# Kernel optimization log

Measured on AMD Instinct MI355X. Metric: run time of the kernel, lower is better.

The kernel has to match this reference:

```python
import jax, jax.numpy as jnp
import numpy as np

GRID_SIZE = 5       # efficient-KAN defaults
SPLINE_ORDER = 3
GRID_RANGE = (-1.0, 1.0)
N_BASIS = GRID_SIZE + SPLINE_ORDER  # 8
LN_EPS = 1e-5


def _make_grid(in_features):
    h = (GRID_RANGE[1] - GRID_RANGE[0]) / GRID_SIZE
    g = np.arange(-SPLINE_ORDER, GRID_SIZE + SPLINE_ORDER + 1, dtype=np.float32) * h + GRID_RANGE[0]
    return jnp.asarray(np.tile(g, (in_features, 1)))  # [in, G+2k+1]


def _b_splines(x, grid):
    # x: [N, in], grid: [in, G+2k+1] -> [N, in, G+k]
    x = x[..., None]
    bases = ((x >= grid[:, :-1]) & (x < grid[:, 1:])).astype(x.dtype)
    for k in range(1, SPLINE_ORDER + 1):
        bases = ((x - grid[:, : -(k + 1)]) / (grid[:, k:-1] - grid[:, : -(k + 1)]) * bases[..., :-1]
                 + (grid[:, k + 1:] - x) / (grid[:, k + 1:] - grid[:, 1:-k]) * bases[..., 1:])
    return bases


def _layer_norm(x, scale, bias):
    mu = jnp.mean(x, axis=-1, keepdims=True)
    var = jnp.mean(jnp.square(x - mu), axis=-1, keepdims=True)
    return (x - mu) * jax.lax.rsqrt(var + LN_EPS) * scale + bias


def setup_inputs() -> dict:
    key = jax.random.key(0)
    B, S, D = 2, 4096, 256
    IN = 3 * D
    ks = jax.random.split(key, 20)
    s = 0.02
    inp = {
        'axial_tokens': jax.random.normal(ks[0], (B, S, D), jnp.float32),
        'sagittal_tokens': jax.random.normal(ks[1], (B, S, D), jnp.float32),
        'coronal_tokens': jax.random.normal(ks[2], (B, S, D), jnp.float32),
        'wq': jax.random.normal(ks[3], (D, D), jnp.float32) * s,
        'bq': jnp.zeros((D,), jnp.float32),
        'wk': jax.random.normal(ks[4], (D, D), jnp.float32) * s,
        'bk': jnp.zeros((D,), jnp.float32),
        'wv': jax.random.normal(ks[5], (D, D), jnp.float32) * s,
        'bv': jnp.zeros((D,), jnp.float32),
        'view_emb': jax.random.normal(ks[6], (3, D), jnp.float32) * s,
        'ln_ax_scale': jnp.ones((D,), jnp.float32), 'ln_ax_bias': jnp.zeros((D,), jnp.float32),
        'ln_sg_scale': jnp.ones((D,), jnp.float32), 'ln_sg_bias': jnp.zeros((D,), jnp.float32),
        'ln_co_scale': jnp.ones((D,), jnp.float32), 'ln_co_bias': jnp.zeros((D,), jnp.float32),
        'base_weight': jax.random.normal(ks[7], (D, IN), jnp.float32) * s,
        'spline_weight': jax.random.normal(ks[8], (D, IN, N_BASIS), jnp.float32) * s,
        'spline_scaler': 1.0 + jax.random.normal(ks[9], (D, IN), jnp.float32) * 0.1,
    }
    return inp


def reference(axial_tokens, sagittal_tokens, coronal_tokens,
              wq, bq, wk, bk, wv, bv, view_emb,
              ln_ax_scale, ln_ax_bias, ln_sg_scale, ln_sg_bias, ln_co_scale, ln_co_bias,
              base_weight, spline_weight, spline_scaler):
    D = axial_tokens.shape[-1]
    inv_sqrt_d = 1.0 / jnp.sqrt(jnp.float32(D))

    def attend(tokens, emb, ln_s, ln_b):
        q = tokens @ wq.T + bq
        k = tokens @ wk.T + bk
        v = tokens @ wv.T + bv
        # torch adds q @ view_emb_row_broadcast^T: every column of the bias equals q . emb
        bias = (q @ emb)[..., None]                      # [B,S,1]
        scores = jnp.einsum('bqd,bkd->bqk', q, k) * inv_sqrt_d + bias
        w = jax.nn.softmax(scores, axis=-1)
        att = jnp.einsum('bqk,bkd->bqd', w, v)
        return _layer_norm(att + tokens, ln_s, ln_b)

    ax = attend(axial_tokens, view_emb[0], ln_ax_scale, ln_ax_bias)
    sg = attend(sagittal_tokens, view_emb[1], ln_sg_scale, ln_sg_bias)
    co = attend(coronal_tokens, view_emb[2], ln_co_scale, ln_co_bias)

    x = jnp.concatenate((ax, sg, co), axis=-1)          # [B,S,3D]
    B, S, IN = x.shape
    grid = _make_grid(IN)
    base = jax.nn.silu(x) @ base_weight.T               # [B,S,D]
    sb = _b_splines(x.reshape(-1, IN), grid)            # [B*S, IN, G+k]
    sw = spline_weight * spline_scaler[..., None]       # [D, IN, G+k]
    spline = jnp.einsum('nif,oif->no', sb, sw).reshape(B, S, -1)
    return base + spline
```

## Files before the change

kernel.cpp:

```cpp
#include <hip/hip_runtime.h>
#include <hip/hip_bf16.h>
#include <math.h>


typedef __hip_bfloat16 bf16;
using bf16x8 = __attribute__((ext_vector_type(8))) __bf16;
using f32x4  = __attribute__((ext_vector_type(4))) float;

__device__ __forceinline__ void load_lds16(const void* g, void* l) {
  __builtin_amdgcn_global_load_lds((__attribute__((address_space(1))) void*)g,
                                   (__attribute__((address_space(3))) void*)l,
                                   16, 0, 0);
}

__device__ __forceinline__ float wave_sum(float v) {
#pragma unroll
  for (int o = 32; o > 0; o >>= 1) v += __shfl_down(v, o, 64);
  return v;
}

template <typename OutT, bool EXP>
__global__ __launch_bounds__(256) void mfma_gemm_bt(
    const bf16* __restrict__ A, const bf16* __restrict__ B,
    const float* __restrict__ bias, OutT* __restrict__ C,
    float* __restrict__ lpart, int K, int lda, int ldb, int ldc, int zshift,
    size_t zAh, size_t zAl, size_t zBh, size_t zBl, size_t zC, float scale) {
  __shared__ __align__(16) bf16 As[4096];
  __shared__ __align__(16) bf16 Bs[4096];
  const int tid = (int)threadIdx.x;
  const int lane = tid & 63;
  const int w = tid >> 6;
  const int m0 = (int)blockIdx.y << 7;
  const int n0 = (int)blockIdx.x << 7;
  const size_t z = blockIdx.z;
  const size_t zlo = z & (((size_t)1 << zshift) - 1);
  A += (z >> zshift) * zAh + zlo * zAl;
  B += (z >> zshift) * zBh + zlo * zBl;
  C += z * zC;

  const int srow = lane >> 2;
  const int qg = (lane & 3) ^ ((lane >> 3) & 3);
  const int ci0 = w, ci1 = w + 4;
  const bf16* gA0 = A + (size_t)(m0 + ci0 * 16 + srow) * lda + qg * 8;
  const bf16* gA1 = A + (size_t)(m0 + ci1 * 16 + srow) * lda + qg * 8;
  const bf16* gB0 = B + (size_t)(n0 + ci0 * 16 + srow) * ldb + qg * 8;
  const bf16* gB1 = B + (size_t)(n0 + ci1 * 16 + srow) * ldb + qg * 8;
  bf16* lA0 = As + ci0 * 512;
  bf16* lA1 = As + ci1 * 512;
  bf16* lB0 = Bs + ci0 * 512;
  bf16* lB1 = Bs + ci1 * 512;

  const int m15 = lane & 15, quad = lane >> 4;
  const int fq = quad ^ ((m15 >> 1) & 3);
  const int aoff = m15 * 32 + fq * 8;
  const bf16* pA = As + ((w >> 1) << 11) + aoff;
  const bf16* pB = Bs + ((w & 1) << 11) + aoff;

  f32x4 acc[4][4];
#pragma unroll
  for (int mi = 0; mi < 4; ++mi)
#pragma unroll
    for (int ni = 0; ni < 4; ++ni) acc[mi][ni] = (f32x4)(0.0f);

  for (int k0 = 0; k0 < K; k0 += 32) {
    load_lds16(gA0, lA0);
    load_lds16(gA1, lA1);
    load_lds16(gB0, lB0);
    load_lds16(gB1, lB1);
    gA0 += 32; gA1 += 32; gB0 += 32; gB1 += 32;
    __syncthreads();
    bf16x8 av[4], bv[4];
#pragma unroll
    for (int i = 0; i < 4; ++i) {
      av[i] = *(const bf16x8*)(pA + i * 512);
      bv[i] = *(const bf16x8*)(pB + i * 512);
    }
#pragma unroll
    for (int mi = 0; mi < 4; ++mi)
#pragma unroll
      for (int ni = 0; ni < 4; ++ni)
        acc[mi][ni] = __builtin_amdgcn_mfma_f32_16x16x32_bf16(
            av[mi], bv[ni], acc[mi][ni], 0, 0, 0);
    __syncthreads();
  }

  const int crow = m0 + ((w >> 1) << 6) + quad * 4;
  const int ccol = n0 + ((w & 1) << 6) + m15;
  float rs[4][4] = {};
#pragma unroll
  for (int ni = 0; ni < 4; ++ni) {
    const int col = ccol + ni * 16;
    const float bb = bias ? bias[col] : 0.0f;
#pragma unroll
    for (int mi = 0; mi < 4; ++mi) {
#pragma unroll
      for (int i = 0; i < 4; ++i) {
        const int row = crow + mi * 16 + i;
        float v = acc[mi][ni][i] * scale + bb;
        if constexpr (EXP) {
          v = __expf(v);
          rs[mi][i] += v;
        }
        if constexpr (sizeof(OutT) == 2)
          C[(size_t)row * ldc + col] = __float2bfloat16(v);
        else
          C[(size_t)row * ldc + col] = v;
      }
    }
  }
  if constexpr (EXP) {
    const int ch = ((int)blockIdx.x << 1) | (w & 1);
#pragma unroll
    for (int mi = 0; mi < 4; ++mi)
#pragma unroll
      for (int i = 0; i < 4; ++i) {
        float sv = rs[mi][i];
        sv += __shfl_xor(sv, 1);
        sv += __shfl_xor(sv, 2);
        sv += __shfl_xor(sv, 4);
        sv += __shfl_xor(sv, 8);
        if (m15 == 0)
          lpart[(size_t)ch * 4096 + crow + mi * 16 + i] = sv;
      }
  }
}

__global__ __launch_bounds__(256) void resid_ln_kernel(
    const float* __restrict__ attp, const float* __restrict__ lpart,
    const float* __restrict__ tok, const float* __restrict__ gamma,
    const float* __restrict__ beta, float* __restrict__ x, int vIdx) {
  __shared__ float red[4];
  __shared__ float sinvl;
  const int n = (int)blockIdx.x;
  const int d = (int)threadIdx.x;
  const int b = n >> 12, r = n & 4095;
  float ls = 0.f;
  if (d < 64) ls = lpart[((size_t)(b * 64 + d)) * 4096 + r];
  ls = wave_sum(ls);
  if (d == 0) sinvl = 1.0f / ls;
  const size_t abase = (size_t)(b * 4) * 1048576 + (size_t)r * 256 + d;
  const float asum = attp[abase] + attp[abase + 1048576] +
                     attp[abase + 2097152] + attp[abase + 3145728];
  __syncthreads();
  const float y = asum * sinvl + tok[(size_t)n * 256 + d];
  float s = wave_sum(y);
  if ((d & 63) == 0) red[d >> 6] = s;
  __syncthreads();
  const float mu = (red[0] + red[1] + red[2] + red[3]) * (1.0f / 256.0f);
  __syncthreads();
  const float c = y - mu;
  float s2 = wave_sum(c * c);
  if ((d & 63) == 0) red[d >> 6] = s2;
  __syncthreads();
  const float var = (red[0] + red[1] + red[2] + red[3]) * (1.0f / 256.0f);
  const float rstd = rsqrtf(var + 1e-5f);
  x[(size_t)n * 768 + vIdx * 256 + d] = c * rstd * gamma[d] + beta[d];
}

__global__ __launch_bounds__(256) void prep_w(
    const float* __restrict__ bw, const float* __restrict__ sw,
    const float* __restrict__ scaler, bf16* __restrict__ Wmat) {
  const int o = blockIdx.x;
  for (int ii = 0; ii < 3; ++ii) {
    const int i = ii * 256 + (int)threadIdx.x;
    const float s = scaler[(size_t)o * 768 + i];
    bf16* p = Wmat + (size_t)o * 6912 + i * 9;
    const float* swp = sw + ((size_t)o * 768 + i) * 8;
#pragma unroll
    for (int f = 0; f < 8; ++f) p[f] = __float2bfloat16(swp[f] * s);
    p[8] = __float2bfloat16(bw[(size_t)o * 768 + i]);
  }
}

__global__ __launch_bounds__(256) void prep_qkvw(
    const float* __restrict__ wq, const float* __restrict__ wk,
    const float* __restrict__ wv, const float* __restrict__ bq,
    const float* __restrict__ bk, const float* __restrict__ bv,
    bf16* __restrict__ wqkvb, float* __restrict__ bqkv) {
  const int idx = blockIdx.x * 256 + (int)threadIdx.x;
  const int row = idx >> 8, col = idx & 255;
  const float* src = row < 256 ? wq : (row < 512 ? wk : wv);
  wqkvb[idx] = __float2bfloat16(src[((row & 255) << 8) + col]);
  if (idx < 768)
    bqkv[idx] = idx < 256 ? bq[idx] : (idx < 512 ? bk[idx - 256] : bv[idx - 512]);
}

__global__ __launch_bounds__(256) void cast_tok3(
    const float4* __restrict__ t0, const float4* __restrict__ t1,
    const float4* __restrict__ t2, bf16* __restrict__ dst) {
  const int vv = blockIdx.y;
  const float4* src = vv == 0 ? t0 : (vv == 1 ? t1 : t2);
  const int idx = blockIdx.x * 256 + (int)threadIdx.x;
  const float4 val = src[idx];
  bf16* p = dst + (size_t)vv * 2097152 + (size_t)idx * 4;
  p[0] = __float2bfloat16(val.x);
  p[1] = __float2bfloat16(val.y);
  p[2] = __float2bfloat16(val.z);
  p[3] = __float2bfloat16(val.w);
}

__global__ __launch_bounds__(256) void transpose_v(
    const bf16* __restrict__ qkv, bf16* __restrict__ vT) {
  __shared__ bf16 tle[64][65];
  const int s0 = blockIdx.x << 6, d0 = blockIdx.y << 6, z = blockIdx.z;
  const int tid = (int)threadIdx.x;
  const int c = tid & 63, rr = tid >> 6;
  for (int r = 0; r < 64; r += 4)
    tle[r + rr][c] = qkv[(size_t)(z * 4096 + s0 + r + rr) * 768 + 512 + d0 + c];
  __syncthreads();
  for (int r = 0; r < 64; r += 4)
    vT[(size_t)z * 1048576 + (size_t)(d0 + r + rr) * 4096 + s0 + c] =
        tle[c][r + rr];
}

__global__ __launch_bounds__(256) void basis_kernel(
    const float* __restrict__ x, bf16* __restrict__ basis) {
  const int i = blockIdx.x * 256 + (int)threadIdx.x;
  const int n = blockIdx.y;
  const float xv = x[(size_t)n * 768 + i];
  float b[11];
#pragma unroll
  for (int m = 0; m < 11; ++m) {
    const float g0 = 0.4f * (float)(m - 3) - 1.0f;
    const float g1 = 0.4f * (float)(m - 2) - 1.0f;
    b[m] = (xv >= g0 && xv < g1) ? 1.0f : 0.0f;
  }
#pragma unroll
  for (int k = 1; k <= 3; ++k) {
    const float inv = 1.0f / (0.4f * (float)k);
#pragma unroll
    for (int m = 0; m + k < 11; ++m) {
      const float gm = 0.4f * (float)(m - 3) - 1.0f;
      const float gmk1 = 0.4f * (float)(m + k - 2) - 1.0f;
      b[m] = (xv - gm) * inv * b[m] + (gmk1 - xv) * inv * b[m + 1];
    }
  }
  bf16* p = basis + (size_t)n * 6912 + i * 9;
#pragma unroll
  for (int f = 0; f < 8; ++f) p[f] = __float2bfloat16(b[f]);
  p[8] = __float2bfloat16(xv / (1.0f + __expf(-xv)));
}

__global__ __launch_bounds__(256) void combine4_kernel(
    const float4* __restrict__ p, float4* __restrict__ out) {
  const int idx = blockIdx.x * 256 + (int)threadIdx.x;
  const float4 a = p[idx];
  const float4 b = p[idx + 524288];
  const float4 c = p[idx + 1048576];
  const float4 d = p[idx + 1572864];
  out[idx] =
      make_float4(a.x + b.x + c.x + d.x, a.y + b.y + c.y + d.y,
                  a.z + b.z + c.z + d.z, a.w + b.w + c.w + d.w);
}

extern "C" void kernel_launch(void* const* d_in, const int* in_sizes, int n_in,
                              void* d_out, int out_size, void* d_ws,
                              size_t ws_size, hipStream_t stream) {
  const float* tok[3] = {(const float*)d_in[0], (const float*)d_in[1],
                         (const float*)d_in[2]};
  const float* wq = (const float*)d_in[3];
  const float* bq = (const float*)d_in[4];
  const float* wk = (const float*)d_in[5];
  const float* bk = (const float*)d_in[6];
  const float* wv = (const float*)d_in[7];
  const float* bv = (const float*)d_in[8];
  const float* lng[3] = {(const float*)d_in[10], (const float*)d_in[12],
                         (const float*)d_in[14]};
  const float* lnb[3] = {(const float*)d_in[11], (const float*)d_in[13],
                         (const float*)d_in[15]};
  const float* bw = (const float*)d_in[16];
  const float* sw = (const float*)d_in[17];
  const float* scaler = (const float*)d_in[18];

  char* w8 = (char*)d_ws;
  bf16* tokb = (bf16*)(w8 + 0);
  bf16* qkv = (bf16*)(w8 + 12582912);
  bf16* vT = (bf16*)(w8 + 50331648);
  bf16* Pb = (bf16*)(w8 + 62914560);
  float* lpart = (float*)(w8 + 130023424);
  float* attp = (float*)(w8 + 132120576);
  float* x = (float*)(w8 + 165675008);
  bf16* Wmat = (bf16*)(w8 + 190840832);
  bf16* wqkvb = (bf16*)(w8 + 194379776);
  float* bqkv = (float*)(w8 + 194772992);
  bf16* basis = (bf16*)(w8 + 0);
  float* pout = attp;

  prep_w<<<256, 256, 0, stream>>>(bw, sw, scaler, Wmat);
  prep_qkvw<<<768, 256, 0, stream>>>(wq, wk, wv, bq, bk, bv, wqkvb, bqkv);
  cast_tok3<<<dim3(2048, 3), 256, 0, stream>>>(
      (const float4*)tok[0], (const float4*)tok[1], (const float4*)tok[2],
      tokb);

  mfma_gemm_bt<bf16, false><<<dim3(6, 192, 1), 256, 0, stream>>>(
      tokb, wqkvb, bqkv, qkv, nullptr, 256, 256, 256, 768, 1, 0, 0, 0, 0, 0,
      1.0f);
  transpose_v<<<dim3(64, 4, 6), 256, 0, stream>>>(qkv, vT);

  for (int v = 0; v < 3; ++v) {
    for (int b = 0; b < 2; ++b) {
      const bf16* qb = qkv + (size_t)(2 * v + b) * 4096 * 768;
      mfma_gemm_bt<bf16, true><<<dim3(32, 32, 1), 256, 0, stream>>>(
          qb, qb + 256, nullptr, Pb + (size_t)b * 16777216,
          lpart + (size_t)b * 262144, 256, 768, 768, 4096, 1, 0, 0, 0, 0, 0,
          0.0625f);
    }
    mfma_gemm_bt<float, false><<<dim3(2, 32, 8), 256, 0, stream>>>(
        Pb, vT + (size_t)(2 * v) * 1048576, nullptr, attp, nullptr, 1024,
        4096, 4096, 256, 2, 16777216, 1024, 1048576, 1024, 1048576, 1.0f);
    resid_ln_kernel<<<8192, 256, 0, stream>>>(attp, lpart, tok[v], lng[v],
                                              lnb[v], x, v);
  }

  basis_kernel<<<dim3(3, 8192), 256, 0, stream>>>(x, basis);
  mfma_gemm_bt<float, false><<<dim3(2, 64, 4), 256, 0, stream>>>(
      basis, Wmat, nullptr, pout, nullptr, 1728, 6912, 6912, 256, 2, 0, 1728,
      0, 1728, 2097152, 1.0f);
  combine4_kernel<<<2048, 256, 0, stream>>>((const float4*)pout,
                                            (float4*)d_out);
}
```

Baseline: 544.7 us.

## Fuse token cast and B-spline basis generation into GEMM A-tile loads

Adds a GEMM variant that reads fp32 activations straight from global memory and builds the bf16 A tile in registers. For the QKV projection it casts tokens on the fly, and for the KAN layer it evaluates a closed-form cubic B-spline or SiLU per element. This removes the separate cast_tok3 and basis_kernel passes and their large intermediate buffers, and Wmat is relaid out basis-major to match. The two per-batch score GEMMs are also merged into one launch via the z dimension. The cost is that the A operand now goes through synchronous register loads with no global-to-LDS async path, and the basis math is recomputed inside the GEMM, once per N-tile.

```diff
diff --git a/kernel.cpp b/kernel.cpp
--- a/kernel.cpp
+++ b/kernel.cpp
@@ -24,7 +24,8 @@
     const bf16* __restrict__ A, const bf16* __restrict__ B,
     const float* __restrict__ bias, OutT* __restrict__ C,
     float* __restrict__ lpart, int K, int lda, int ldb, int ldc, int zshift,
-    size_t zAh, size_t zAl, size_t zBh, size_t zBl, size_t zC, float scale) {
+    size_t zAh, size_t zAl, size_t zBh, size_t zBl, size_t zC, size_t zL,
+    float scale) {
   __shared__ __align__(16) bf16 As[4096];
   __shared__ __align__(16) bf16 Bs[4096];
   const int tid = (int)threadIdx.x;
@@ -37,6 +38,7 @@
   A += (z >> zshift) * zAh + zlo * zAl;
   B += (z >> zshift) * zBh + zlo * zBl;
   C += z * zC;
+  if (EXP) lpart += z * zL;
 
   const int srow = lane >> 2;
   const int qg = (lane & 3) ^ ((lane >> 3) & 3);
@@ -122,6 +124,148 @@
         if (m15 == 0)
           lpart[(size_t)ch * 4096 + crow + mi * 16 + i] = sv;
       }
+  }
+}
+
+template <int GEN, typename OutT>
+__global__ __launch_bounds__(256) void mfma_gemm_genA(
+    const float* __restrict__ X0, const float* __restrict__ X1,
+    const float* __restrict__ X2, int ldx, const bf16* __restrict__ B,
+    const float* __restrict__ bias, OutT* __restrict__ C, int Kslice,
+    int ldb, int ldc, int zshift, size_t zBl, size_t zC, float scale) {
+  __shared__ __align__(16) bf16 As[4096];
+  __shared__ __align__(16) bf16 Bs[4096];
+  const int tid = (int)threadIdx.x;
+  const int lane = tid & 63;
+  const int w = tid >> 6;
+  const int m0 = (int)blockIdx.y << 7;
+  const int n0 = (int)blockIdx.x << 7;
+  const size_t z = blockIdx.z;
+  const size_t zlo = z & (((size_t)1 << zshift) - 1);
+  B += zlo * zBl;
+  C += z * zC;
+  const int kofs = (int)zlo * Kslice;
+
+  const int srow = lane >> 2;
+  const int qg = (lane & 3) ^ ((lane >> 3) & 3);
+  const bf16* gB0 = B + (size_t)(n0 + w * 16 + srow) * ldb + qg * 8;
+  const bf16* gB1 = B + (size_t)(n0 + (w + 4) * 16 + srow) * ldb + qg * 8;
+  bf16* lB0 = Bs + w * 512;
+  bf16* lB1 = Bs + (w + 4) * 512;
+
+  const int arow = tid >> 1;
+  const int seg = (tid & 1) << 4;
+  const int swz = ((arow & 15) >> 1) & 3;
+  const int g0 = seg >> 3;
+  bf16* aw0 = As + arow * 32 + ((g0 ^ swz) << 3);
+  bf16* aw1 = As + arow * 32 + (((g0 + 1) ^ swz) << 3);
+  const float* Xp;
+  if constexpr (GEN == 1) {
+    const int v = m0 >> 13;
+    const float* Xs = v == 0 ? X0 : (v == 1 ? X1 : X2);
+    Xp = Xs + (size_t)((m0 & 8191) + arow) * ldx + seg;
+  } else {
+    Xp = X0 + (size_t)(m0 + arow) * ldx + seg;
+  }
+  int f = kofs / 768;
+  int ib = kofs - f * 768;
+
+  const int m15 = lane & 15, quad = lane >> 4;
+  const int fqA = quad ^ ((m15 >> 1) & 3);
+  const int aoff = m15 * 32 + fqA * 8;
+  const bf16* pA = As + ((w >> 1) << 11) + aoff;
+  const bf16* pB = Bs + ((w & 1) << 11) + aoff;
+
+  f32x4 acc[4][4];
+#pragma unroll
+  for (int mi = 0; mi < 4; ++mi)
+#pragma unroll
+    for (int ni = 0; ni < 4; ++ni) acc[mi][ni] = (f32x4)(0.0f);
+
+  for (int k0 = 0; k0 < Kslice; k0 += 32) {
+    load_lds16(gB0, lB0);
+    load_lds16(gB1, lB1);
+    gB0 += 32; gB1 += 32;
+
+    const float* xs = Xp + ib;
+    const float4 q0 = *(const float4*)(xs);
+    const float4 q1 = *(const float4*)(xs + 4);
+    const float4 q2 = *(const float4*)(xs + 8);
+    const float4 q3 = *(const float4*)(xs + 12);
+    float xv[16] = {q0.x, q0.y, q0.z, q0.w, q1.x, q1.y, q1.z, q1.w,
+                    q2.x, q2.y, q2.z, q2.w, q3.x, q3.y, q3.z, q3.w};
+    union { bf16x8 v; bf16 e[8]; } u0, u1;
+    if constexpr (GEN == 1) {
+#pragma unroll
+      for (int j = 0; j < 8; ++j) {
+        u0.e[j] = __float2bfloat16(xv[j]);
+        u1.e[j] = __float2bfloat16(xv[8 + j]);
+      }
+    } else {
+      if (f < 8) {
+        const float tofs = 5.5f - (float)f;
+#pragma unroll
+        for (int j = 0; j < 16; ++j) {
+          const float t = fmaf(xv[j], 2.5f, tofs);
+          const float tc = fminf(fmaxf(t, 0.0f), 4.0f);
+          const float p2 = fmaxf(tc - 1.0f, 0.0f);
+          const float p3 = fmaxf(tc - 2.0f, 0.0f);
+          const float p4 = fmaxf(tc - 3.0f, 0.0f);
+          const float val = (tc * tc * tc - 4.0f * p2 * p2 * p2 +
+                             6.0f * p3 * p3 * p3 - 4.0f * p4 * p4 * p4) *
+                            (1.0f / 6.0f);
+          if (j < 8) u0.e[j] = __float2bfloat16(val);
+          else u1.e[j - 8] = __float2bfloat16(val);
+        }
+      } else {
+#pragma unroll
+        for (int j = 0; j < 16; ++j) {
+          const float val = xv[j] / (1.0f + __expf(-xv[j]));
+          if (j < 8) u0.e[j] = __float2bfloat16(val);
+          else u1.e[j - 8] = __float2bfloat16(val);
+        }
+      }
+    }
+    *(bf16x8*)aw0 = u0.v;
+    *(bf16x8*)aw1 = u1.v;
+
+    __syncthreads();
+    bf16x8 av[4], bv[4];
+#pragma unroll
+    for (int i = 0; i < 4; ++i) {
+      av[i] = *(const bf16x8*)(pA + i * 512);
+      bv[i] = *(const bf16x8*)(pB + i * 512);
+    }
+#pragma unroll
+    for (int mi = 0; mi < 4; ++mi)
+#pragma unroll
+      for (int ni = 0; ni < 4; ++ni)
+        acc[mi][ni] = __builtin_amdgcn_mfma_f32_16x16x32_bf16(
+            av[mi], bv[ni], acc[mi][ni], 0, 0, 0);
+    __syncthreads();
+
+    ib += 32;
+    if (ib == 768) { ib = 0; ++f; }
+  }
+
+  const int crow = m0 + ((w >> 1) << 6) + quad * 4;
+  const int ccol = n0 + ((w & 1) << 6) + m15;
+#pragma unroll
+  for (int ni = 0; ni < 4; ++ni) {
+    const int col = ccol + ni * 16;
+    const float bb = bias ? bias[col] : 0.0f;
+#pragma unroll
+    for (int mi = 0; mi < 4; ++mi) {
+#pragma unroll
+      for (int i = 0; i < 4; ++i) {
+        const int row = crow + mi * 16 + i;
+        const float v = acc[mi][ni][i] * scale + bb;
+        if constexpr (sizeof(OutT) == 2)
+          C[(size_t)row * ldc + col] = __float2bfloat16(v);
+        else
+          C[(size_t)row * ldc + col] = v;
+      }
+    }
   }
 }
 
@@ -161,14 +305,14 @@
     const float* __restrict__ bw, const float* __restrict__ sw,
     const float* __restrict__ scaler, bf16* __restrict__ Wmat) {
   const int o = blockIdx.x;
+  bf16* p = Wmat + (size_t)o * 6912;
   for (int ii = 0; ii < 3; ++ii) {
     const int i = ii * 256 + (int)threadIdx.x;
     const float s = scaler[(size_t)o * 768 + i];
-    bf16* p = Wmat + (size_t)o * 6912 + i * 9;
     const float* swp = sw + ((size_t)o * 768 + i) * 8;
 #pragma unroll
-    for (int f = 0; f < 8; ++f) p[f] = __float2bfloat16(swp[f] * s);
-    p[8] = __float2bfloat16(bw[(size_t)o * 768 + i]);
+    for (int f = 0; f < 8; ++f) p[f * 768 + i] = __float2bfloat16(swp[f] * s);
+    p[6144 + i] = __float2bfloat16(bw[(size_t)o * 768 + i]);
   }
 }
 
@@ -183,20 +327,6 @@
   wqkvb[idx] = __float2bfloat16(src[((row & 255) << 8) + col]);
   if (idx < 768)
     bqkv[idx] = idx < 256 ? bq[idx] : (idx < 512 ? bk[idx - 256] : bv[idx - 512]);
-}
-
-__global__ __launch_bounds__(256) void cast_tok3(
-    const float4* __restrict__ t0, const float4* __restrict__ t1,
-    const float4* __restrict__ t2, bf16* __restrict__ dst) {
-  const int vv = blockIdx.y;
-  const float4* src = vv == 0 ? t0 : (vv == 1 ? t1 : t2);
-  const int idx = blockIdx.x * 256 + (int)threadIdx.x;
-  const float4 val = src[idx];
-  bf16* p = dst + (size_t)vv * 2097152 + (size_t)idx * 4;
-  p[0] = __float2bfloat16(val.x);
-  p[1] = __float2bfloat16(val.y);
-  p[2] = __float2bfloat16(val.z);
-  p[3] = __float2bfloat16(val.w);
 }
 
 __global__ __launch_bounds__(256) void transpose_v(
@@ -211,34 +341,6 @@
   for (int r = 0; r < 64; r += 4)
     vT[(size_t)z * 1048576 + (size_t)(d0 + r + rr) * 4096 + s0 + c] =
         tle[c][r + rr];
-}
-
-__global__ __launch_bounds__(256) void basis_kernel(
-    const float* __restrict__ x, bf16* __restrict__ basis) {
-  const int i = blockIdx.x * 256 + (int)threadIdx.x;
-  const int n = blockIdx.y;
-  const float xv = x[(size_t)n * 768 + i];
-  float b[11];
-#pragma unroll
-  for (int m = 0; m < 11; ++m) {
-    const float g0 = 0.4f * (float)(m - 3) - 1.0f;
-    const float g1 = 0.4f * (float)(m - 2) - 1.0f;
-    b[m] = (xv >= g0 && xv < g1) ? 1.0f : 0.0f;
-  }
-#pragma unroll
-  for (int k = 1; k <= 3; ++k) {
-    const float inv = 1.0f / (0.4f * (float)k);
-#pragma unroll
-    for (int m = 0; m + k < 11; ++m) {
-      const float gm = 0.4f * (float)(m - 3) - 1.0f;
-      const float gmk1 = 0.4f * (float)(m + k - 2) - 1.0f;
-      b[m] = (xv - gm) * inv * b[m] + (gmk1 - xv) * inv * b[m + 1];
-    }
-  }
-  bf16* p = basis + (size_t)n * 6912 + i * 9;
-#pragma unroll
-  for (int f = 0; f < 8; ++f) p[f] = __float2bfloat16(b[f]);
-  p[8] = __float2bfloat16(xv / (1.0f + __expf(-xv)));
 }
 
 __global__ __launch_bounds__(256) void combine4_kernel(
@@ -273,49 +375,40 @@
   const float* scaler = (const float*)d_in[18];
 
   char* w8 = (char*)d_ws;
-  bf16* tokb = (bf16*)(w8 + 0);
-  bf16* qkv = (bf16*)(w8 + 12582912);
-  bf16* vT = (bf16*)(w8 + 50331648);
-  bf16* Pb = (bf16*)(w8 + 62914560);
-  float* lpart = (float*)(w8 + 130023424);
-  float* attp = (float*)(w8 + 132120576);
-  float* x = (float*)(w8 + 165675008);
-  bf16* Wmat = (bf16*)(w8 + 190840832);
-  bf16* wqkvb = (bf16*)(w8 + 194379776);
-  float* bqkv = (float*)(w8 + 194772992);
-  bf16* basis = (bf16*)(w8 + 0);
+  bf16* qkv = (bf16*)(w8 + 0);
+  bf16* vT = (bf16*)(w8 + 37748736);
+  bf16* Pb = (bf16*)(w8 + 50331648);
+  float* lpart = (float*)(w8 + 117440512);
+  float* attp = (float*)(w8 + 119537664);
+  float* x = (float*)(w8 + 153092096);
+  bf16* Wmat = (bf16*)(w8 + 178257920);
+  bf16* wqkvb = (bf16*)(w8 + 181796864);
+  float* bqkv = (float*)(w8 + 182190080);
   float* pout = attp;
 
   prep_w<<<256, 256, 0, stream>>>(bw, sw, scaler, Wmat);
   prep_qkvw<<<768, 256, 0, stream>>>(wq, wk, wv, bq, bk, bv, wqkvb, bqkv);
-  cast_tok3<<<dim3(2048, 3), 256, 0, stream>>>(
-      (const float4*)tok[0], (const float4*)tok[1], (const float4*)tok[2],
-      tokb);
-
-  mfma_gemm_bt<bf16, false><<<dim3(6, 192, 1), 256, 0, stream>>>(
-      tokb, wqkvb, bqkv, qkv, nullptr, 256, 256, 256, 768, 1, 0, 0, 0, 0, 0,
+
+  mfma_gemm_genA<1, bf16><<<dim3(6, 192, 1), 256, 0, stream>>>(
+      tok[0], tok[1], tok[2], 256, wqkvb, bqkv, qkv, 256, 256, 768, 0, 0, 0,
       1.0f);
   transpose_v<<<dim3(64, 4, 6), 256, 0, stream>>>(qkv, vT);
 
   for (int v = 0; v < 3; ++v) {
-    for (int b = 0; b < 2; ++b) {
-      const bf16* qb = qkv + (size_t)(2 * v + b) * 4096 * 768;
-      mfma_gemm_bt<bf16, true><<<dim3(32, 32, 1), 256, 0, stream>>>(
-          qb, qb + 256, nullptr, Pb + (size_t)b * 16777216,
-          lpart + (size_t)b * 262144, 256, 768, 768, 4096, 1, 0, 0, 0, 0, 0,
-          0.0625f);
-    }
+    const bf16* qb = qkv + (size_t)(2 * v) * 4096 * 768;
+    mfma_gemm_bt<bf16, true><<<dim3(32, 32, 2), 256, 0, stream>>>(
+        qb, qb + 256, nullptr, Pb, lpart, 256, 768, 768, 4096, 1, 0, 3145728,
+        0, 3145728, 16777216, 262144, 0.0625f);
     mfma_gemm_bt<float, false><<<dim3(2, 32, 8), 256, 0, stream>>>(
         Pb, vT + (size_t)(2 * v) * 1048576, nullptr, attp, nullptr, 1024,
-        4096, 4096, 256, 2, 16777216, 1024, 1048576, 1024, 1048576, 1.0f);
+        4096, 4096, 256, 2, 16777216, 1024, 1048576, 1024, 1048576, 0, 1.0f);
     resid_ln_kernel<<<8192, 256, 0, stream>>>(attp, lpart, tok[v], lng[v],
                                               lnb[v], x, v);
   }
 
-  basis_kernel<<<dim3(3, 8192), 256, 0, stream>>>(x, basis);
-  mfma_gemm_bt<float, false><<<dim3(2, 64, 4), 256, 0, stream>>>(
-      basis, Wmat, nullptr, pout, nullptr, 1728, 6912, 6912, 256, 2, 0, 1728,
-      0, 1728, 2097152, 1.0f);
+  mfma_gemm_genA<2, float><<<dim3(2, 64, 4), 256, 0, stream>>>(
+      x, x, x, 768, Wmat, nullptr, pout, 1728, 6912, 256, 2, 1728, 2097152,
+      1.0f);
   combine4_kernel<<<2048, 256, 0, stream>>>((const float4*)pout,
                                             (float4*)d_out);
 }
```

New measurement: 545.9 us. No clear change (+0.2%).

## Fuse B-spline basis generation into residual LayerNorm and batch score GEMMs

Applied to the files above, without the earlier changes.

The residual+LayerNorm kernel now evaluates the cubic B-spline bases in closed form (a clamped truncated-power formula) plus SiLU, and writes the bf16 basis row directly. This removes the separate basis kernel and the fp32 x round trip. The two per-batch score GEMM launches are merged into one launch with a z dimension, using a new lpart stride argument. The fused path needs a larger workspace, so it runs only when ws_size is big enough and otherwise falls back to the old path.

```diff
diff --git a/kernel.cpp b/kernel.cpp
--- a/kernel.cpp
+++ b/kernel.cpp
@@ -17,6 +17,16 @@
 #pragma unroll
   for (int o = 32; o > 0; o >>= 1) v += __shfl_down(v, o, 64);
   return v;
+}
+
+__device__ __forceinline__ float b3_cardinal(float x, float tofs) {
+  const float t = fmaf(x, 2.5f, tofs);
+  const float tc = fminf(fmaxf(t, 0.0f), 4.0f);
+  const float p2 = fmaxf(tc - 1.0f, 0.0f);
+  const float p3 = fmaxf(tc - 2.0f, 0.0f);
+  const float p4 = fmaxf(tc - 3.0f, 0.0f);
+  return (tc * tc * tc - 4.0f * p2 * p2 * p2 + 6.0f * p3 * p3 * p3 -
+          4.0f * p4 * p4 * p4) * (1.0f / 6.0f);
 }
 
 template <typename OutT, bool EXP>
@@ -24,7 +34,8 @@
     const bf16* __restrict__ A, const bf16* __restrict__ B,
     const float* __restrict__ bias, OutT* __restrict__ C,
     float* __restrict__ lpart, int K, int lda, int ldb, int ldc, int zshift,
-    size_t zAh, size_t zAl, size_t zBh, size_t zBl, size_t zC, float scale) {
+    size_t zAh, size_t zAl, size_t zBh, size_t zBl, size_t zC, size_t zL,
+    float scale) {
   __shared__ __align__(16) bf16 As[4096];
   __shared__ __align__(16) bf16 Bs[4096];
   const int tid = (int)threadIdx.x;
@@ -37,6 +48,7 @@
   A += (z >> zshift) * zAh + zlo * zAl;
   B += (z >> zshift) * zBh + zlo * zBl;
   C += z * zC;
+  if (EXP) lpart += z * zL;
 
   const int srow = lane >> 2;
   const int qg = (lane & 3) ^ ((lane >> 3) & 3);
@@ -125,12 +137,15 @@
   }
 }
 
+template <bool FUSE>
 __global__ __launch_bounds__(256) void resid_ln_kernel(
     const float* __restrict__ attp, const float* __restrict__ lpart,
     const float* __restrict__ tok, const float* __restrict__ gamma,
-    const float* __restrict__ beta, float* __restrict__ x, int vIdx) {
+    const float* __restrict__ beta, float* __restrict__ xout,
+    bf16* __restrict__ basis, int vIdx) {
   __shared__ float red[4];
   __shared__ float sinvl;
+  __shared__ __align__(16) bf16 st[2304];
   const int n = (int)blockIdx.x;
   const int d = (int)threadIdx.x;
   const int b = n >> 12, r = n & 4095;
@@ -154,7 +169,20 @@
   __syncthreads();
   const float var = (red[0] + red[1] + red[2] + red[3]) * (1.0f / 256.0f);
   const float rstd = rsqrtf(var + 1e-5f);
-  x[(size_t)n * 768 + vIdx * 256 + d] = c * rstd * gamma[d] + beta[d];
+  const float val = c * rstd * gamma[d] + beta[d];
+  if constexpr (!FUSE) {
+    xout[(size_t)n * 768 + vIdx * 256 + d] = val;
+  } else {
+#pragma unroll
+    for (int f = 0; f < 8; ++f)
+      st[d * 9 + f] = __float2bfloat16(b3_cardinal(val, 5.5f - (float)f));
+    st[d * 9 + 8] = __float2bfloat16(val / (1.0f + __expf(-val)));
+    __syncthreads();
+    float4* gb = (float4*)((char*)basis + (size_t)n * 13824 + vIdx * 4608);
+    const float4* sb = (const float4*)st;
+    gb[d] = sb[d];
+    if (d < 32) gb[256 + d] = sb[256 + d];
+  }
 }
 
 __global__ __launch_bounds__(256) void prep_w(
@@ -272,6 +300,7 @@
   const float* sw = (const float*)d_in[17];
   const float* scaler = (const float*)d_in[18];
 
+  const bool fused = ws_size >= 282856448ull;
   char* w8 = (char*)d_ws;
   bf16* tokb = (bf16*)(w8 + 0);
   bf16* qkv = (bf16*)(w8 + 12582912);
@@ -279,12 +308,21 @@
   bf16* Pb = (bf16*)(w8 + 62914560);
   float* lpart = (float*)(w8 + 130023424);
   float* attp = (float*)(w8 + 132120576);
-  float* x = (float*)(w8 + 165675008);
-  bf16* Wmat = (bf16*)(w8 + 190840832);
-  bf16* wqkvb = (bf16*)(w8 + 194379776);
-  float* bqkv = (float*)(w8 + 194772992);
-  bf16* basis = (bf16*)(w8 + 0);
   float* pout = attp;
+  float* x;
+  bf16* basis;
+  bf16* Wmat;
+  if (fused) {
+    x = nullptr;
+    basis = (bf16*)(w8 + 165675008);
+    Wmat = (bf16*)(w8 + 278921216);
+  } else {
+    x = (float*)(w8 + 165675008);
+    basis = (bf16*)(w8 + 0);
+    Wmat = (bf16*)(w8 + 190840832);
+  }
+  bf16* wqkvb = (bf16*)((char*)Wmat + 3538944);
+  float* bqkv = (float*)((char*)wqkvb + 393216);
 
   prep_w<<<256, 256, 0, stream>>>(bw, sw, scaler, Wmat);
   prep_qkvw<<<768, 256, 0, stream>>>(wq, wk, wv, bq, bk, bv, wqkvb, bqkv);
@@ -294,28 +332,30 @@
 
   mfma_gemm_bt<bf16, false><<<dim3(6, 192, 1), 256, 0, stream>>>(
       tokb, wqkvb, bqkv, qkv, nullptr, 256, 256, 256, 768, 1, 0, 0, 0, 0, 0,
-      1.0f);
+      0, 1.0f);
   transpose_v<<<dim3(64, 4, 6), 256, 0, stream>>>(qkv, vT);
 
   for (int v = 0; v < 3; ++v) {
-    for (int b = 0; b < 2; ++b) {
-      const bf16* qb = qkv + (size_t)(2 * v + b) * 4096 * 768;
-      mfma_gemm_bt<bf16, true><<<dim3(32, 32, 1), 256, 0, stream>>>(
-          qb, qb + 256, nullptr, Pb + (size_t)b * 16777216,
-          lpart + (size_t)b * 262144, 256, 768, 768, 4096, 1, 0, 0, 0, 0, 0,
-          0.0625f);
-    }
+    const bf16* qb = qkv + (size_t)(2 * v) * 4096 * 768;
+    mfma_gemm_bt<bf16, true><<<dim3(32, 32, 2), 256, 0, stream>>>(
+        qb, qb + 256, nullptr, Pb, lpart, 256, 768, 768, 4096, 1, 0, 3145728,
+        0, 3145728, 16777216, 262144, 0.0625f);
     mfma_gemm_bt<float, false><<<dim3(2, 32, 8), 256, 0, stream>>>(
         Pb, vT + (size_t)(2 * v) * 1048576, nullptr, attp, nullptr, 1024,
-        4096, 4096, 256, 2, 16777216, 1024, 1048576, 1024, 1048576, 1.0f);
-    resid_ln_kernel<<<8192, 256, 0, stream>>>(attp, lpart, tok[v], lng[v],
-                                              lnb[v], x, v);
-  }
-
-  basis_kernel<<<dim3(3, 8192), 256, 0, stream>>>(x, basis);
+        4096, 4096, 256, 2, 16777216, 1024, 1048576, 1024, 1048576, 0, 1.0f);
+    if (fused)
+      resid_ln_kernel<true><<<8192, 256, 0, stream>>>(
+          attp, lpart, tok[v], lng[v], lnb[v], nullptr, basis, v);
+    else
+      resid_ln_kernel<false><<<8192, 256, 0, stream>>>(
+          attp, lpart, tok[v], lng[v], lnb[v], x, nullptr, v);
+  }
+
+  if (!fused) basis_kernel<<<dim3(3, 8192), 256, 0, stream>>>(x, basis);
+
   mfma_gemm_bt<float, false><<<dim3(2, 64, 4), 256, 0, stream>>>(
       basis, Wmat, nullptr, pout, nullptr, 1728, 6912, 6912, 256, 2, 0, 1728,
-      0, 1728, 2097152, 1.0f);
+      0, 1728, 2097152, 0, 1.0f);
   combine4_kernel<<<2048, 256, 0, stream>>>((const float4*)pout,
                                             (float4*)d_out);
 }
```

After: 528.7 us. 2.9% less time.
